# Performance work log

Measured on AMD Instinct MI355X. Metric: run time of the kernel, lower is better.

## Reference

```python
import jax, jax.numpy as jnp
import numpy as np

B, N, C, H, AD, HID = 2, 1024, 768, 12, 8, 3072
SCALE = (C // H) ** -0.5


def setup_inputs() -> dict:
    key = jax.random.key(0)
    ks = jax.random.split(key, 32)
    inp = {}
    for i in range(5):
        inp[f"x{i}"] = jax.random.normal(ks[i], (B, N, C), jnp.float32)
    def w(i, shape, s=0.02):
        return jax.random.normal(ks[i], shape, jnp.float32) * s
    inp.update({
        "ln1_g": jnp.ones((C,), jnp.float32), "ln1_b": jnp.zeros((C,), jnp.float32),
        "ln2_g": jnp.ones((C,), jnp.float32), "ln2_b": jnp.zeros((C,), jnp.float32),
        "qkv_w": w(5, (C, 3 * C)), "qkv_b": jnp.zeros((3 * C,), jnp.float32),
        "proj_w": w(6, (C, C)), "proj_b": jnp.zeros((C,), jnp.float32),
        "fc1_w": w(7, (C, HID)), "fc1_b": jnp.zeros((HID,), jnp.float32),
        "fc2_w": w(8, (HID, C)), "fc2_b": jnp.zeros((C,), jnp.float32),
        "at_dw": w(9, (C, AD)), "at_db": jnp.zeros((AD,), jnp.float32),
        "at_mw": w(10, (AD, AD)), "at_mb": jnp.zeros((AD,), jnp.float32),
        "at_uw": w(11, (AD, C)), "at_ub": jnp.zeros((C,), jnp.float32),
        "a2_dw": w(12, (C, AD)), "a2_db": jnp.zeros((AD,), jnp.float32),
        "a2_mw": w(13, (AD, AD)), "a2_mb": jnp.zeros((AD,), jnp.float32),
        "a2_uw": w(14, (AD, C)), "a2_ub": jnp.zeros((C,), jnp.float32),
    })
    return inp


def _ln(x, g, b, eps=1e-5):
    mu = x.mean(-1, keepdims=True)
    xc = x - mu
    var = (xc * xc).mean(-1, keepdims=True)
    return xc * jax.lax.rsqrt(var + eps) * g + b


def _adapter(x, dw, db, mw, mb, uw, ub):
    h = x @ dw + db          # bottleneck down [., AD]
    h = h @ mw + mb          # mid
    return h @ uw + ub       # up back to C


def _attn(x, qkv_w, qkv_b, proj_w, proj_b):
    # x: [S, B, N, C] (streams folded in leading axis)
    s, b, n, c = x.shape
    qkv = (x @ qkv_w + qkv_b).reshape(s, b, n, 3, H, c // H)
    q, k, v = jnp.moveaxis(qkv, 3, 0)            # each [S,B,N,H,D]
    scores = jnp.einsum('sbnhd,sbmhd->sbhnm', q * SCALE, k)  # fp32; clamp is a no-op
    p = jax.nn.softmax(scores, axis=-1)
    o = jnp.einsum('sbhnm,sbmhd->sbnhd', p, v).reshape(s, b, n, c)
    return o @ proj_w + proj_b


def reference(x0, x1, x2, x3, x4,
              ln1_g, ln1_b, ln2_g, ln2_b,
              qkv_w, qkv_b, proj_w, proj_b,
              fc1_w, fc1_b, fc2_w, fc2_b,
              at_dw, at_db, at_mw, at_mb, at_uw, at_ub,
              a2_dw, a2_db, a2_mw, a2_mb, a2_uw, a2_ub):
    xs = jnp.stack([x0, x1, x2, x3, x4])          # [5,B,N,C]
    n1 = _ln(xs, ln1_g, ln1_b)
    a1 = _adapter(n1, at_dw, at_db, at_mw, at_mb, at_uw, at_ub)
    ao = _attn(n1, qkv_w, qkv_b, proj_w, proj_b)
    # cross-stream residuals: x01=a1[0], x12=a1[1], ..., x10=a1[1], x21=a1[2], ...
    y0 = xs[0] + ao[0] + a1[1]
    y1 = xs[1] + ao[1] + a1[0] + a1[2]
    y2 = xs[2] + ao[2] + a1[1] + a1[3]
    y3 = xs[3] + ao[3] + a1[2] + a1[4]
    y4 = xs[4] + ao[4] + a1[3]
    ys = jnp.stack([y0, y1, y2, y3, y4])
    a2 = _adapter(_ln(ys, ln1_g, ln1_b), a2_dw, a2_db, a2_mw, a2_mb, a2_uw, a2_ub)
    h = _ln(ys, ln2_g, ln2_b) @ fc1_w + fc1_b
    m = jax.nn.gelu(h, approximate=False) @ fc2_w + fc2_b
    z0 = ys[0] + m[0] + a2[1]
    z1 = ys[1] + m[1] + a2[0] + a2[2]
    z2 = ys[2] + m[2] + a2[1] + a2[3]
    z3 = ys[3] + m[3] + a2[2] + a2[4]
    z4 = ys[4] + m[4] + a2[3]
    return jnp.stack([z0, z1, z2, z3, z4])        # [5,B,N,C]
```

## Files before the change

kernel.cpp:

```cpp
#include <hip/hip_runtime.h>
#include <math.h>

typedef __bf16 bf16;
typedef __attribute__((ext_vector_type(8))) __bf16 bf16x8;
typedef __attribute__((ext_vector_type(4))) __bf16 bf16x4;
typedef __attribute__((ext_vector_type(4))) float f32x4;
typedef __attribute__((ext_vector_type(16))) float f32x16;

#define TOK   10240
#define CD    768
#define NQKV  2304
#define NHID  3072
#define SEQ   1024
#define NH    12

__device__ __forceinline__ f32x4 mfma16(bf16x8 a, bf16x8 b, f32x4 c) {
  return __builtin_amdgcn_mfma_f32_16x16x32_bf16(a, b, c, 0, 0, 0);
}
__device__ __forceinline__ f32x16 mfma32(bf16x8 a, bf16x8 b, f32x16 c) {
  return __builtin_amdgcn_mfma_f32_32x32x16_bf16(a, b, c, 0, 0, 0);
}

__device__ __forceinline__ void gload16(const void* g, void* l) {
  __builtin_amdgcn_global_load_lds(
      (const __attribute__((address_space(1))) void*)g,
      (__attribute__((address_space(3))) void*)l, 16, 0, 0);
}

__device__ __forceinline__ unsigned pack2(bf16 a, bf16 b) {
  union { unsigned short u[2]; unsigned v; } x;
  x.u[0] = __builtin_bit_cast(unsigned short, a);
  x.u[1] = __builtin_bit_cast(unsigned short, b);
  return x.v;
}

__device__ __forceinline__ f32x4 b4tof(const bf16* p) {
  bf16x4 v = *(const bf16x4*)p;
  f32x4 r;
#pragma unroll
  for (int j = 0; j < 4; ++j) r[j] = (float)v[j];
  return r;
}

__device__ __forceinline__ float fast_gelu(float v) {
  float u = 0.7978845608f * (v + 0.044715f * v * v * v);
  float e = __expf(fminf(2.f * u, 30.f));
  return 0.5f * v * (1.f + (e - 1.f) / (e + 1.f));
}

__global__ __launch_bounds__(256) void transpose_to_bf16(
    const float* __restrict__ in, bf16* __restrict__ out, int K, int N) {
  __shared__ float tile[32][33];
  const int bn = blockIdx.x * 32, bk = blockIdx.y * 32;
  const int r = threadIdx.x >> 5, c = threadIdx.x & 31;
#pragma unroll
  for (int i = 0; i < 4; ++i)
    tile[r + 8 * i][c] = in[(size_t)(bk + r + 8 * i) * N + bn + c];
  __syncthreads();
#pragma unroll
  for (int i = 0; i < 4; ++i)
    out[(size_t)(bn + r + 8 * i) * K + bk + c] = (bf16)tile[c][r + 8 * i];
}

__global__ __launch_bounds__(256) void ln5_kernel(
    const float* __restrict__ x0, const float* __restrict__ x1,
    const float* __restrict__ x2, const float* __restrict__ x3,
    const float* __restrict__ x4, const float* __restrict__ g,
    const float* __restrict__ b, bf16* __restrict__ out) {
  const int w = threadIdx.x >> 6, lane = threadIdx.x & 63;
  const int row = blockIdx.x * 4 + w;
  const int s = row >> 11, rem = row & 2047;
  const float* xp;
  switch (s) {
    case 0: xp = x0; break; case 1: xp = x1; break; case 2: xp = x2; break;
    case 3: xp = x3; break; default: xp = x4; break;
  }
  const f32x4* xr = (const f32x4*)(xp + (size_t)rem * CD);
  f32x4 v[3];
#pragma unroll
  for (int i = 0; i < 3; ++i) v[i] = xr[lane + 64 * i];
  float sum = 0.f;
#pragma unroll
  for (int i = 0; i < 3; ++i)
#pragma unroll
    for (int j = 0; j < 4; ++j) sum += v[i][j];
#pragma unroll
  for (int m = 32; m >= 1; m >>= 1) sum += __shfl_xor(sum, m);
  const float mu = sum * (1.f / 768.f);
  float vs = 0.f;
#pragma unroll
  for (int i = 0; i < 3; ++i)
#pragma unroll
    for (int j = 0; j < 4; ++j) { float d = v[i][j] - mu; vs += d * d; }
#pragma unroll
  for (int m = 32; m >= 1; m >>= 1) vs += __shfl_xor(vs, m);
  const float rstd = rsqrtf(vs * (1.f / 768.f) + 1e-5f);
  const f32x4* gp = (const f32x4*)g;
  const f32x4* bp = (const f32x4*)b;
  bf16* orow = out + (size_t)row * CD;
#pragma unroll
  for (int i = 0; i < 3; ++i) {
    const int c4 = lane + 64 * i;
    f32x4 gg = gp[c4], bb = bp[c4];
    bf16x4 o;
#pragma unroll
    for (int j = 0; j < 4; ++j)
      o[j] = (bf16)((v[i][j] - mu) * rstd * gg[j] + bb[j]);
    *(bf16x4*)(orow + c4 * 4) = o;
  }
}

__global__ __launch_bounds__(256) void fuse_res_ln(
    const float* __restrict__ x0, const float* __restrict__ x1,
    const float* __restrict__ x2, const float* __restrict__ x3,
    const float* __restrict__ x4, const float* __restrict__ add,
    const bf16* __restrict__ a, float* __restrict__ ys,
    const float* __restrict__ g1, const float* __restrict__ b1,
    const float* __restrict__ g2, const float* __restrict__ b2,
    bf16* __restrict__ o1, bf16* __restrict__ o2) {
  const int w = threadIdx.x >> 6, lane = threadIdx.x & 63;
  const int row = blockIdx.x * 4 + w;
  const int s = row >> 11, rem = row & 2047;
  const float* xp;
  switch (s) {
    case 0: xp = x0; break; case 1: xp = x1; break; case 2: xp = x2; break;
    case 3: xp = x3; break; default: xp = x4; break;
  }
  const f32x4* xr = (const f32x4*)(xp + (size_t)rem * CD);
  const f32x4* ar = (const f32x4*)(add + (size_t)row * CD);
  const bf16* am = a + (size_t)(row - 2048) * CD;
  const bf16* ap = a + (size_t)(row + 2048) * CD;
  f32x4 v[3];
#pragma unroll
  for (int i = 0; i < 3; ++i) {
    const int c4 = lane + 64 * i;
    f32x4 t = xr[c4] + ar[c4];
    if (s > 0) t += b4tof(am + c4 * 4);
    if (s < 4) t += b4tof(ap + c4 * 4);
    v[i] = t;
  }
  f32x4* yr = (f32x4*)(ys + (size_t)row * CD);
#pragma unroll
  for (int i = 0; i < 3; ++i) yr[lane + 64 * i] = v[i];

  float sum = 0.f;
#pragma unroll
  for (int i = 0; i < 3; ++i)
#pragma unroll
    for (int j = 0; j < 4; ++j) sum += v[i][j];
#pragma unroll
  for (int m = 32; m >= 1; m >>= 1) sum += __shfl_xor(sum, m);
  const float mu = sum * (1.f / 768.f);
  float vs = 0.f;
#pragma unroll
  for (int i = 0; i < 3; ++i)
#pragma unroll
    for (int j = 0; j < 4; ++j) { float d = v[i][j] - mu; vs += d * d; }
#pragma unroll
  for (int m = 32; m >= 1; m >>= 1) vs += __shfl_xor(vs, m);
  const float rstd = rsqrtf(vs * (1.f / 768.f) + 1e-5f);
  bf16* r1 = o1 + (size_t)row * CD;
  bf16* r2 = o2 + (size_t)row * CD;
#pragma unroll
  for (int i = 0; i < 3; ++i) {
    const int c4 = lane + 64 * i;
    f32x4 gg1 = ((const f32x4*)g1)[c4], bb1 = ((const f32x4*)b1)[c4];
    f32x4 gg2 = ((const f32x4*)g2)[c4], bb2 = ((const f32x4*)b2)[c4];
    bf16x4 oa, ob;
#pragma unroll
    for (int j = 0; j < 4; ++j) {
      float n = (v[i][j] - mu) * rstd;
      oa[j] = (bf16)(n * gg1[j] + bb1[j]);
      ob[j] = (bf16)(n * gg2[j] + bb2[j]);
    }
    *(bf16x4*)(r1 + c4 * 4) = oa;
    *(bf16x4*)(r2 + c4 * 4) = ob;
  }
}

#define GBAR() __builtin_amdgcn_s_barrier()

#define LOADA(MH, BUF)                                                      \
  _Pragma("unroll") for (int m_ = 0; m_ < 4; ++m_) {                        \
    af[m_][0] =                                                             \
        *(const bf16x8*)&As[BUF][((MH)*128 + arow + m_ * 16) * 64 + ach0];  \
    af[m_][1] =                                                             \
        *(const bf16x8*)&As[BUF][((MH)*128 + arow + m_ * 16) * 64 + ach1];  \
  }

#define LOADB(DST, NH, BUF)                                                 \
  _Pragma("unroll") for (int n_ = 0; n_ < 2; ++n_) {                        \
    DST[n_][0] =                                                            \
        *(const bf16x8*)&Bs[BUF][(brow + (NH)*32 + n_ * 16) * 64 + ach0];   \
    DST[n_][1] =                                                            \
        *(const bf16x8*)&Bs[BUF][(brow + (NH)*32 + n_ * 16) * 64 + ach1];   \
  }

#define MFMA_PH(MH, NH, BF)                                                 \
  __builtin_amdgcn_s_setprio(1);                                            \
  _Pragma("unroll") for (int m_ = 0; m_ < 4; ++m_)                          \
  _Pragma("unroll") for (int n_ = 0; n_ < 2; ++n_) {                        \
    acc[(MH)*4 + m_][(NH)*2 + n_] =                                         \
        mfma16(af[m_][0], BF[n_][0], acc[(MH)*4 + m_][(NH)*2 + n_]);        \
    acc[(MH)*4 + m_][(NH)*2 + n_] =                                         \
        mfma16(af[m_][1], BF[n_][1], acc[(MH)*4 + m_][(NH)*2 + n_]);        \
  }                                                                         \
  __builtin_amdgcn_s_setprio(0);

template <int EPI>
__global__ __launch_bounds__(512, 2) void gemm256(
    const bf16* __restrict__ A, const bf16* __restrict__ Bt,
    const float* __restrict__ bias, void* __restrict__ Cout, int N, int Klen,
    int ldk, int nbn, int bpk, size_t kpstride) {
  __shared__ bf16 As[2][16384];
  __shared__ bf16 Bs[2][16384];
  const int t = threadIdx.x, lane = t & 63, w = t >> 6;
  const int wm = w >> 2, wn = w & 3;

  const int chunkg = gridDim.x >> 3;
  const int wg = (blockIdx.x & 7) * chunkg + (blockIdx.x >> 3);
  const int kp = wg / bpk, rem = wg % bpk;
  const int bm = rem / nbn, bn = rem % nbn;

  f32x4 acc[8][4] = {};

  const int srow = t >> 3;
  const int scol = ((t & 7) ^ (srow & 7)) << 3;
  const size_t koff = (size_t)kp * Klen;
  const bf16* Ab = A + (size_t)(bm * 256 + srow) * ldk + koff + scol;
  const bf16* Bb = Bt + (size_t)(bn * 256 + srow) * ldk + koff + scol;
  const size_t r64 = (size_t)64 * ldk;

  auto stage_a = [&](int buf, int h, int kt) {
    const bf16* g = Ab + (size_t)h * 128 * ldk + (size_t)kt * 64;
    gload16(g, &As[buf][h * 8192 + w * 512]);
    gload16(g + r64, &As[buf][h * 8192 + 4096 + w * 512]);
  };
  auto stage_b = [&](int buf, int h, int kt) {
    const bf16* g = Bb + (size_t)h * 128 * ldk + (size_t)kt * 64;
    gload16(g, &Bs[buf][h * 8192 + w * 512]);
    gload16(g + r64, &Bs[buf][h * 8192 + 4096 + w * 512]);
  };

  const int arow = wm * 64 + (lane & 15);
  const int brow = wn * 64 + (lane & 15);
  const int ach0 = (((lane >> 4) + 0) ^ (lane & 7)) << 3;
  const int ach1 = (((lane >> 4) + 4) ^ (lane & 7)) << 3;

  stage_a(0, 0, 0); stage_b(0, 0, 0); stage_b(0, 1, 0); stage_a(0, 1, 0);
  stage_a(1, 0, 1); stage_b(1, 0, 1);
  asm volatile("s_waitcnt vmcnt(4)" ::: "memory");
  GBAR();

  const int NT = Klen >> 6, NI = NT >> 1;
  bf16x8 af[4][2], bf0[2][2], bf1[2][2];

  for (int j = 0; j < NI; ++j) {
    const int tA = 2 * j, tB = 2 * j + 1;
    const bool notlast = (j + 1 < NI);

    LOADA(0, 0);
    LOADB(bf0, 0, 0);
    stage_b(1, 1, tB);
    GBAR();
    MFMA_PH(0, 0, bf0);
    GBAR();
    LOADB(bf1, 1, 0);
    stage_a(1, 1, tB);
    GBAR();
    MFMA_PH(0, 1, bf1);
    GBAR();
    LOADA(1, 0);
    if (notlast) stage_a(0, 0, tA + 2);
    GBAR();
    MFMA_PH(1, 0, bf0);
    GBAR();
    if (notlast) {
      stage_b(0, 0, tA + 2);
      asm volatile("s_waitcnt vmcnt(4)" ::: "memory");
    } else {
      asm volatile("s_waitcnt vmcnt(0)" ::: "memory");
    }
    GBAR();
    MFMA_PH(1, 1, bf1);
    GBAR();

    LOADA(0, 1);
    LOADB(bf0, 0, 1);
    if (notlast) stage_b(0, 1, tA + 2);
    GBAR();
    MFMA_PH(0, 0, bf0);
    GBAR();
    LOADB(bf1, 1, 1);
    if (notlast) stage_a(0, 1, tA + 2);
    GBAR();
    MFMA_PH(0, 1, bf1);
    GBAR();
    LOADA(1, 1);
    if (notlast) stage_a(1, 0, tB + 2);
    GBAR();
    MFMA_PH(1, 0, bf0);
    GBAR();
    if (notlast) {
      stage_b(1, 0, tB + 2);
      asm volatile("s_waitcnt vmcnt(4)" ::: "memory");
    }
    GBAR();
    MFMA_PH(1, 1, bf1);
    GBAR();
  }

#pragma unroll
  for (int am = 0; am < 8; ++am) {
    const int grow0 =
        bm * 256 + (am >> 2) * 128 + wm * 64 + (am & 3) * 16 + (lane >> 4) * 4;
#pragma unroll
    for (int an = 0; an < 4; ++an) {
      const int gcol = bn * 256 + wn * 64 + an * 16 + (lane & 15);
      const float bv = (kp == 0) ? bias[gcol] : 0.f;
#pragma unroll
      for (int r = 0; r < 4; ++r) {
        float v = acc[am][an][r] + bv;
        if (EPI == 2) v = fast_gelu(v);
        const size_t idx = (size_t)(grow0 + r) * N + gcol + kp * kpstride;
        if (EPI == 0) ((float*)Cout)[idx] = v;
        else ((bf16*)Cout)[idx] = (bf16)v;
      }
    }
  }
}

__global__ __launch_bounds__(256, 3) void attn_v2(
    const bf16* __restrict__ qkv, bf16* __restrict__ obuf) {
  __shared__ bf16 Ks[2][4096];
  __shared__ bf16 Vt[2][4096];
  const int t = threadIdx.x, lane = t & 63, w = t >> 6;
  const int g = lane >> 5, q32 = lane & 31, rq7 = q32 & 7;

  const int xcd = blockIdx.x & 7, slot = blockIdx.x >> 3;
  const int work = xcd * 120 + slot;
  const int sbh = work >> 3, qt = work & 7;
  const int sb = sbh / NH, h = sbh % NH;
  const size_t tokbase = (size_t)sb * SEQ;
  const int qoff = h * 64, koff = CD + h * 64, voff = 2 * CD + h * 64;

  const int qrow = qt * 128 + w * 32 + q32;
  bf16x8 qf[4];
  {
    const bf16* qp = qkv + (tokbase + qrow) * NQKV + qoff + g * 8;
#pragma unroll
    for (int kd = 0; kd < 4; ++kd) {
      bf16x8 v = *(const bf16x8*)(qp + kd * 16);
#pragma unroll
      for (int j = 0; j < 8; ++j) v[j] = (bf16)((float)v[j] * 0.125f);
      qf[kd] = v;
    }
  }

  const int skv1 = t >> 3, sc1 = (t & 7) ^ (skv1 & 7);
  const int skv2 = (t + 256) >> 3, sc2 = (t & 7) ^ (skv2 & 7);
  const int vkv0 = 2 * (t & 31);
  const int vd0 = 8 * (t >> 5);
  const int c0 = (vkv0 & 51) | ((vkv0 & 4) << 1) | ((vkv0 & 8) >> 1);
  const int vchunk = c0 >> 3, vsub = c0 & 7;
  const bf16* kbase = qkv + tokbase * NQKV + koff;
  const bf16* vbase = qkv + tokbase * NQKV + voff;

  {
    const bf16* kb0 = kbase;
    gload16(kb0 + (size_t)skv1 * NQKV + sc1 * 8, &Ks[0][w * 512]);
    gload16(kb0 + (size_t)skv2 * NQKV + sc2 * 8, &Ks[0][2048 + w * 512]);
    const bf16* vp = vbase + (size_t)vkv0 * NQKV + vd0;
    bf16x8 r0 = *(const bf16x8*)vp;
    bf16x8 r1 = *(const bf16x8*)(vp + NQKV);
#pragma unroll
    for (int j = 0; j < 8; ++j) {
      const int d = vd0 + j;
      *(unsigned*)&Vt[0][d * 64 + ((vchunk ^ j) << 3) + vsub] =
          pack2(r0[j], r1[j]);
    }
  }
  __syncthreads();

  float m_run = -1e30f, l_run = 0.f;
  f32x16 oT0 = {}, oT1 = {};
  int cur = 0;

  for (int kt = 0; kt < 16; ++kt) {
    bf16x8 nv0, nv1;
    if (kt < 15) {
      const bf16* vp = vbase + (size_t)((kt + 1) * 64 + vkv0) * NQKV + vd0;
      nv0 = *(const bf16x8*)vp;
      nv1 = *(const bf16x8*)(vp + NQKV);
      const bf16* kb0 = kbase + (size_t)(kt + 1) * 64 * NQKV;
      gload16(kb0 + (size_t)skv1 * NQKV + sc1 * 8, &Ks[cur ^ 1][w * 512]);
      gload16(kb0 + (size_t)skv2 * NQKV + sc2 * 8,
              &Ks[cur ^ 1][2048 + w * 512]);
    }

    f32x16 sT0 = {}, sT1 = {};
#pragma unroll
    for (int kd = 0; kd < 4; ++kd) {
      bf16x8 kf0 =
          *(const bf16x8*)&Ks[cur][q32 * 64 + (((2 * kd + g) ^ rq7) << 3)];
      bf16x8 kf1 = *(const bf16x8*)&Ks[cur][(32 + q32) * 64 +
                                            (((2 * kd + g) ^ rq7) << 3)];
      sT0 = mfma32(kf0, qf[kd], sT0);
      sT1 = mfma32(kf1, qf[kd], sT1);
    }

    float mt = sT0[0];
#pragma unroll
    for (int r = 1; r < 16; ++r) mt = fmaxf(mt, sT0[r]);
#pragma unroll
    for (int r = 0; r < 16; ++r) mt = fmaxf(mt, sT1[r]);
    mt = fmaxf(mt, __shfl_xor(mt, 32));
    const float mnew = fmaxf(m_run, mt);
    const float alpha = __expf(m_run - mnew);
    m_run = mnew;
    float rs = 0.f;
#pragma unroll
    for (int r = 0; r < 16; ++r) {
      sT0[r] = __expf(sT0[r] - mnew);
      rs += sT0[r];
    }
#pragma unroll
    for (int r = 0; r < 16; ++r) {
      sT1[r] = __expf(sT1[r] - mnew);
      rs += sT1[r];
    }
    rs += __shfl_xor(rs, 32);
    l_run = l_run * alpha + rs;
#pragma unroll
    for (int r = 0; r < 16; ++r) { oT0[r] *= alpha; oT1[r] *= alpha; }

    bf16x8 pa[4];
#pragma unroll
    for (int hh = 0; hh < 2; ++hh)
#pragma unroll
      for (int j = 0; j < 8; ++j) {
        pa[hh][j] = (bf16)sT0[8 * hh + j];
        pa[2 + hh][j] = (bf16)sT1[8 * hh + j];
      }

#pragma unroll
    for (int ks = 0; ks < 4; ++ks) {
      bf16x8 vf0 =
          *(const bf16x8*)&Vt[cur][q32 * 64 + (((2 * ks + g) ^ rq7) << 3)];
      bf16x8 vf1 = *(const bf16x8*)&Vt[cur][(32 + q32) * 64 +
                                            (((2 * ks + g) ^ rq7) << 3)];
      oT0 = mfma32(vf0, pa[ks], oT0);
      oT1 = mfma32(vf1, pa[ks], oT1);
    }

    if (kt < 15) {
#pragma unroll
      for (int j = 0; j < 8; ++j) {
        const int d = vd0 + j;
        *(unsigned*)&Vt[cur ^ 1][d * 64 + ((vchunk ^ j) << 3) + vsub] =
            pack2(nv0[j], nv1[j]);
      }
    }
    __syncthreads();
    cur ^= 1;
  }

  const float rl = 1.f / l_run;
  bf16* orow = obuf + (tokbase + qrow) * CD + h * 64;
#pragma unroll
  for (int m = 0; m < 4; ++m) {
    bf16x4 o0, o1;
#pragma unroll
    for (int r = 0; r < 4; ++r) {
      o0[r] = (bf16)(oT0[4 * m + r] * rl);
      o1[r] = (bf16)(oT1[4 * m + r] * rl);
    }
    *(bf16x4*)(orow + 8 * m + 4 * g) = o0;
    *(bf16x4*)(orow + 32 + 8 * m + 4 * g) = o1;
  }
}

__global__ __launch_bounds__(256) void adapter_kernel(
    const bf16* __restrict__ X, const float* __restrict__ dw,
    const float* __restrict__ db, const float* __restrict__ mw,
    const float* __restrict__ mb, const float* __restrict__ uw,
    const float* __restrict__ ub, bf16* __restrict__ out) {
  const int tok = blockIdx.x * 4 + (threadIdx.x >> 6);
  const int lane = threadIdx.x & 63;
  const bf16* xr = X + (size_t)tok * CD;
  float xv[12];
#pragma unroll
  for (int i = 0; i < 12; ++i) xv[i] = (float)xr[lane + 64 * i];
  float h1[8] = {0, 0, 0, 0, 0, 0, 0, 0};
#pragma unroll
  for (int i = 0; i < 12; ++i) {
    const f32x4* dr = (const f32x4*)(dw + (size_t)(lane + 64 * i) * 8);
    f32x4 d0 = dr[0], d1 = dr[1];
#pragma unroll
    for (int j = 0; j < 4; ++j) {
      h1[j] += xv[i] * d0[j];
      h1[4 + j] += xv[i] * d1[j];
    }
  }
#pragma unroll
  for (int m = 1; m < 64; m <<= 1)
#pragma unroll
    for (int j = 0; j < 8; ++j) h1[j] += __shfl_xor(h1[j], m);
#pragma unroll
  for (int j = 0; j < 8; ++j) h1[j] += db[j];
  float h2[8];
#pragma unroll
  for (int k = 0; k < 8; ++k) {
    float v = mb[k];
#pragma unroll
    for (int j = 0; j < 8; ++j) v += h1[j] * mw[j * 8 + k];
    h2[k] = v;
  }
#pragma unroll
  for (int i = 0; i < 12; ++i) {
    const int c = lane + 64 * i;
    float v = ub[c];
#pragma unroll
    for (int k = 0; k < 8; ++k) v += h2[k] * uw[k * CD + c];
    out[(size_t)tok * CD + c] = (bf16)v;
  }
}

__global__ __launch_bounds__(256) void cross_residual(
    const float* __restrict__ ys, const bf16* __restrict__ m01,
    const bf16* __restrict__ a, float* __restrict__ out) {
  const int s = blockIdx.y;
  const size_t i = (size_t)blockIdx.x * 256 + threadIdx.x;
  const size_t spitch = (size_t)2048 * 768 / 4;
  const size_t sb = (size_t)s * spitch;
  const size_t mstride = (size_t)TOK * CD / 4;
  f32x4 v = ((const f32x4*)ys)[sb + i];
  v += b4tof(m01 + (sb + i) * 4);
  v += b4tof(m01 + (mstride + sb + i) * 4);
  if (s > 0) v += b4tof(a + (sb - spitch + i) * 4);
  if (s < 4) v += b4tof(a + (sb + spitch + i) * 4);
  ((f32x4*)out)[sb + i] = v;
}

#define OFF_WTQKV  ((size_t)0)
#define OFF_WTPROJ ((size_t)3538944)
#define OFF_WTFC1  ((size_t)4718592)
#define OFF_WTFC2  ((size_t)9437184)
#define OFF_N1     ((size_t)14155776)
#define OFF_BIG    ((size_t)29884416)
#define OFF_OBUF   ((size_t)77070336)
#define OFF_AOM    ((size_t)92798976)
#define OFF_A12    ((size_t)124256256)
#define OFF_YS     ((size_t)155713536)
#define OFF_L2Y    ((size_t)187170816)

extern "C" void kernel_launch(void* const* d_in, const int* in_sizes, int n_in,
                              void* d_out, int out_size, void* d_ws,
                              size_t ws_size, hipStream_t stream) {
  const float* x0 = (const float*)d_in[0];
  const float* x1 = (const float*)d_in[1];
  const float* x2 = (const float*)d_in[2];
  const float* x3 = (const float*)d_in[3];
  const float* x4 = (const float*)d_in[4];
  const float* ln1_g = (const float*)d_in[5];
  const float* ln1_b = (const float*)d_in[6];
  const float* ln2_g = (const float*)d_in[7];
  const float* ln2_b = (const float*)d_in[8];
  const float* qkv_w = (const float*)d_in[9];
  const float* qkv_b = (const float*)d_in[10];
  const float* proj_w = (const float*)d_in[11];
  const float* proj_b = (const float*)d_in[12];
  const float* fc1_w = (const float*)d_in[13];
  const float* fc1_b = (const float*)d_in[14];
  const float* fc2_w = (const float*)d_in[15];
  const float* fc2_b = (const float*)d_in[16];
  const float* at_dw = (const float*)d_in[17];
  const float* at_db = (const float*)d_in[18];
  const float* at_mw = (const float*)d_in[19];
  const float* at_mb = (const float*)d_in[20];
  const float* at_uw = (const float*)d_in[21];
  const float* at_ub = (const float*)d_in[22];
  const float* a2_dw = (const float*)d_in[23];
  const float* a2_db = (const float*)d_in[24];
  const float* a2_mw = (const float*)d_in[25];
  const float* a2_mb = (const float*)d_in[26];
  const float* a2_uw = (const float*)d_in[27];
  const float* a2_ub = (const float*)d_in[28];

  char* ws = (char*)d_ws;
  bf16* wt_qkv = (bf16*)(ws + OFF_WTQKV);
  bf16* wt_proj = (bf16*)(ws + OFF_WTPROJ);
  bf16* wt_fc1 = (bf16*)(ws + OFF_WTFC1);
  bf16* wt_fc2 = (bf16*)(ws + OFF_WTFC2);
  bf16* n1 = (bf16*)(ws + OFF_N1);
  bf16* qkvb = (bf16*)(ws + OFF_BIG);
  bf16* obuf = (bf16*)(ws + OFF_OBUF);
  float* aof = (float*)(ws + OFF_AOM);
  bf16* mbuf = (bf16*)(ws + OFF_AOM);
  bf16* a12 = (bf16*)(ws + OFF_A12);
  float* ysb = (float*)(ws + OFF_YS);
  bf16* l2y = (bf16*)(ws + OFF_L2Y);

  const dim3 b256(256);
  const dim3 b512(512);

  transpose_to_bf16<<<dim3(72, 24), b256, 0, stream>>>(qkv_w, wt_qkv, 768, 2304);
  transpose_to_bf16<<<dim3(24, 24), b256, 0, stream>>>(proj_w, wt_proj, 768, 768);
  transpose_to_bf16<<<dim3(96, 24), b256, 0, stream>>>(fc1_w, wt_fc1, 768, 3072);
  transpose_to_bf16<<<dim3(24, 96), b256, 0, stream>>>(fc2_w, wt_fc2, 3072, 768);

  ln5_kernel<<<2560, b256, 0, stream>>>(x0, x1, x2, x3, x4, ln1_g, ln1_b, n1);

  gemm256<1><<<360, b512, 0, stream>>>(n1, wt_qkv, qkv_b, qkvb, NQKV, 768, 768,
                                       9, 360, 0);

  adapter_kernel<<<2560, b256, 0, stream>>>(n1, at_dw, at_db, at_mw, at_mb,
                                            at_uw, at_ub, a12);

  attn_v2<<<960, b256, 0, stream>>>(qkvb, obuf);

  gemm256<0><<<120, b512, 0, stream>>>(obuf, wt_proj, proj_b, aof, CD, 768,
                                       768, 3, 120, 0);

  fuse_res_ln<<<2560, b256, 0, stream>>>(x0, x1, x2, x3, x4, aof, a12, ysb,
                                         ln1_g, ln1_b, ln2_g, ln2_b, n1, l2y);

  adapter_kernel<<<2560, b256, 0, stream>>>(n1, a2_dw, a2_db, a2_mw, a2_mb,
                                            a2_uw, a2_ub, a12);

  gemm256<2><<<480, b512, 0, stream>>>(l2y, wt_fc1, fc1_b, qkvb, NHID, 768,
                                       768, 12, 480, 0);

  gemm256<1><<<240, b512, 0, stream>>>(qkvb, wt_fc2, fc2_b, mbuf, CD, 1536,
                                       3072, 3, 120, (size_t)TOK * CD);

  cross_residual<<<dim3(1536, 5), b256, 0, stream>>>(ysb, mbuf, a12,
                                                     (float*)d_out);
}
```

Measured before the change: 382.9 us.

## Simplify GEMM to K=32 double-buffered loop and split-K the projection GEMM

Replaces the hand-interleaved 8-phase GEMM main loop, which used K=64 tiles and many barriers, with a simpler loop using K=32 tiles and a double buffer. Each step loads all A and B fragments, waits, prefetches the tile two steps ahead, then issues 32 MFMAs, and LDS use is halved. The output projection GEMM now uses split-K over 240 blocks and writes two bf16 partial outputs instead of one fp32 output. The fused residual+LN kernel sums the two bf16 partials, which should fill more CUs but adds bf16 rounding on the projection output. The simpler loop also risks less overlap between loads and MFMA.

```diff
diff --git a/kernel.cpp b/kernel.cpp
--- a/kernel.cpp
+++ b/kernel.cpp
@@ -113,7 +113,7 @@
 __global__ __launch_bounds__(256) void fuse_res_ln(
     const float* __restrict__ x0, const float* __restrict__ x1,
     const float* __restrict__ x2, const float* __restrict__ x3,
-    const float* __restrict__ x4, const float* __restrict__ add,
+    const float* __restrict__ x4, const bf16* __restrict__ m01,
     const bf16* __restrict__ a, float* __restrict__ ys,
     const float* __restrict__ g1, const float* __restrict__ b1,
     const float* __restrict__ g2, const float* __restrict__ b2,
@@ -127,14 +127,15 @@
     case 3: xp = x3; break; default: xp = x4; break;
   }
   const f32x4* xr = (const f32x4*)(xp + (size_t)rem * CD);
-  const f32x4* ar = (const f32x4*)(add + (size_t)row * CD);
+  const bf16* p0 = m01 + (size_t)row * CD;
+  const bf16* p1 = m01 + (size_t)TOK * CD + (size_t)row * CD;
   const bf16* am = a + (size_t)(row - 2048) * CD;
   const bf16* ap = a + (size_t)(row + 2048) * CD;
   f32x4 v[3];
 #pragma unroll
   for (int i = 0; i < 3; ++i) {
     const int c4 = lane + 64 * i;
-    f32x4 t = xr[c4] + ar[c4];
+    f32x4 t = xr[c4] + b4tof(p0 + c4 * 4) + b4tof(p1 + c4 * 4);
     if (s > 0) t += b4tof(am + c4 * 4);
     if (s < 4) t += b4tof(ap + c4 * 4);
     v[i] = t;
@@ -178,42 +179,13 @@
   }
 }
 
-#define GBAR() __builtin_amdgcn_s_barrier()
-
-#define LOADA(MH, BUF)                                                      \
-  _Pragma("unroll") for (int m_ = 0; m_ < 4; ++m_) {                        \
-    af[m_][0] =                                                             \
-        *(const bf16x8*)&As[BUF][((MH)*128 + arow + m_ * 16) * 64 + ach0];  \
-    af[m_][1] =                                                             \
-        *(const bf16x8*)&As[BUF][((MH)*128 + arow + m_ * 16) * 64 + ach1];  \
-  }
-
-#define LOADB(DST, NH, BUF)                                                 \
-  _Pragma("unroll") for (int n_ = 0; n_ < 2; ++n_) {                        \
-    DST[n_][0] =                                                            \
-        *(const bf16x8*)&Bs[BUF][(brow + (NH)*32 + n_ * 16) * 64 + ach0];   \
-    DST[n_][1] =                                                            \
-        *(const bf16x8*)&Bs[BUF][(brow + (NH)*32 + n_ * 16) * 64 + ach1];   \
-  }
-
-#define MFMA_PH(MH, NH, BF)                                                 \
-  __builtin_amdgcn_s_setprio(1);                                            \
-  _Pragma("unroll") for (int m_ = 0; m_ < 4; ++m_)                          \
-  _Pragma("unroll") for (int n_ = 0; n_ < 2; ++n_) {                        \
-    acc[(MH)*4 + m_][(NH)*2 + n_] =                                         \
-        mfma16(af[m_][0], BF[n_][0], acc[(MH)*4 + m_][(NH)*2 + n_]);        \
-    acc[(MH)*4 + m_][(NH)*2 + n_] =                                         \
-        mfma16(af[m_][1], BF[n_][1], acc[(MH)*4 + m_][(NH)*2 + n_]);        \
-  }                                                                         \
-  __builtin_amdgcn_s_setprio(0);
-
 template <int EPI>
 __global__ __launch_bounds__(512, 2) void gemm256(
     const bf16* __restrict__ A, const bf16* __restrict__ Bt,
     const float* __restrict__ bias, void* __restrict__ Cout, int N, int Klen,
     int ldk, int nbn, int bpk, size_t kpstride) {
-  __shared__ bf16 As[2][16384];
-  __shared__ bf16 Bs[2][16384];
+  __shared__ bf16 As[2][8192];
+  __shared__ bf16 Bs[2][8192];
   const int t = threadIdx.x, lane = t & 63, w = t >> 6;
   const int wm = w >> 2, wn = w & 3;
 
@@ -224,103 +196,70 @@
 
   f32x4 acc[8][4] = {};
 
-  const int srow = t >> 3;
-  const int scol = ((t & 7) ^ (srow & 7)) << 3;
+  const int srow = t >> 2;
+  const int scol = ((t & 3) ^ ((srow >> 1) & 3)) << 3;
   const size_t koff = (size_t)kp * Klen;
   const bf16* Ab = A + (size_t)(bm * 256 + srow) * ldk + koff + scol;
   const bf16* Bb = Bt + (size_t)(bn * 256 + srow) * ldk + koff + scol;
-  const size_t r64 = (size_t)64 * ldk;
-
-  auto stage_a = [&](int buf, int h, int kt) {
-    const bf16* g = Ab + (size_t)h * 128 * ldk + (size_t)kt * 64;
-    gload16(g, &As[buf][h * 8192 + w * 512]);
-    gload16(g + r64, &As[buf][h * 8192 + 4096 + w * 512]);
+  const size_t r128 = (size_t)128 * ldk;
+
+  auto stage = [&](int buf, int kt) {
+    const bf16* ga = Ab + (size_t)kt * 32;
+    const bf16* gb = Bb + (size_t)kt * 32;
+    gload16(ga, &As[buf][w * 512]);
+    gload16(ga + r128, &As[buf][4096 + w * 512]);
+    gload16(gb, &Bs[buf][w * 512]);
+    gload16(gb + r128, &Bs[buf][4096 + w * 512]);
   };
-  auto stage_b = [&](int buf, int h, int kt) {
-    const bf16* g = Bb + (size_t)h * 128 * ldk + (size_t)kt * 64;
-    gload16(g, &Bs[buf][h * 8192 + w * 512]);
-    gload16(g + r64, &Bs[buf][h * 8192 + 4096 + w * 512]);
-  };
-
-  const int arow = wm * 64 + (lane & 15);
+
+  const int arow = wm * 128 + (lane & 15);
   const int brow = wn * 64 + (lane & 15);
-  const int ach0 = (((lane >> 4) + 0) ^ (lane & 7)) << 3;
-  const int ach1 = (((lane >> 4) + 4) ^ (lane & 7)) << 3;
-
-  stage_a(0, 0, 0); stage_b(0, 0, 0); stage_b(0, 1, 0); stage_a(0, 1, 0);
-  stage_a(1, 0, 1); stage_b(1, 0, 1);
+  const int achn = (((lane >> 4) ^ ((lane >> 1) & 3)) << 3);
+
+  stage(0, 0);
+  stage(1, 1);
   asm volatile("s_waitcnt vmcnt(4)" ::: "memory");
-  GBAR();
-
-  const int NT = Klen >> 6, NI = NT >> 1;
-  bf16x8 af[4][2], bf0[2][2], bf1[2][2];
-
-  for (int j = 0; j < NI; ++j) {
-    const int tA = 2 * j, tB = 2 * j + 1;
-    const bool notlast = (j + 1 < NI);
-
-    LOADA(0, 0);
-    LOADB(bf0, 0, 0);
-    stage_b(1, 1, tB);
-    GBAR();
-    MFMA_PH(0, 0, bf0);
-    GBAR();
-    LOADB(bf1, 1, 0);
-    stage_a(1, 1, tB);
-    GBAR();
-    MFMA_PH(0, 1, bf1);
-    GBAR();
-    LOADA(1, 0);
-    if (notlast) stage_a(0, 0, tA + 2);
-    GBAR();
-    MFMA_PH(1, 0, bf0);
-    GBAR();
-    if (notlast) {
-      stage_b(0, 0, tA + 2);
+  __builtin_amdgcn_s_barrier();
+
+  const int NT = Klen >> 5;
+  bf16x8 af[8], bfr[4];
+
+  for (int kt = 0; kt < NT; ++kt) {
+    const int buf = kt & 1;
+#pragma unroll
+    for (int m_ = 0; m_ < 8; ++m_)
+      af[m_] = *(const bf16x8*)&As[buf][(arow + m_ * 16) * 32 + achn];
+#pragma unroll
+    for (int n_ = 0; n_ < 4; ++n_)
+      bfr[n_] = *(const bf16x8*)&Bs[buf][(brow + n_ * 16) * 32 + achn];
+    asm volatile("s_waitcnt lgkmcnt(0)" ::: "memory");
+    __builtin_amdgcn_s_barrier();
+    if (kt + 2 < NT) {
+      stage(buf, kt + 2);
       asm volatile("s_waitcnt vmcnt(4)" ::: "memory");
     } else {
       asm volatile("s_waitcnt vmcnt(0)" ::: "memory");
     }
-    GBAR();
-    MFMA_PH(1, 1, bf1);
-    GBAR();
-
-    LOADA(0, 1);
-    LOADB(bf0, 0, 1);
-    if (notlast) stage_b(0, 1, tA + 2);
-    GBAR();
-    MFMA_PH(0, 0, bf0);
-    GBAR();
-    LOADB(bf1, 1, 1);
-    if (notlast) stage_a(0, 1, tA + 2);
-    GBAR();
-    MFMA_PH(0, 1, bf1);
-    GBAR();
-    LOADA(1, 1);
-    if (notlast) stage_a(1, 0, tB + 2);
-    GBAR();
-    MFMA_PH(1, 0, bf0);
-    GBAR();
-    if (notlast) {
-      stage_b(1, 0, tB + 2);
-      asm volatile("s_waitcnt vmcnt(4)" ::: "memory");
-    }
-    GBAR();
-    MFMA_PH(1, 1, bf1);
-    GBAR();
-  }
-
-#pragma unroll
-  for (int am = 0; am < 8; ++am) {
-    const int grow0 =
-        bm * 256 + (am >> 2) * 128 + wm * 64 + (am & 3) * 16 + (lane >> 4) * 4;
-#pragma unroll
-    for (int an = 0; an < 4; ++an) {
-      const int gcol = bn * 256 + wn * 64 + an * 16 + (lane & 15);
+    __builtin_amdgcn_s_barrier();
+    __builtin_amdgcn_s_setprio(1);
+#pragma unroll
+    for (int m_ = 0; m_ < 8; ++m_)
+#pragma unroll
+      for (int n_ = 0; n_ < 4; ++n_)
+        acc[m_][n_] = mfma16(af[m_], bfr[n_], acc[m_][n_]);
+    __builtin_amdgcn_s_setprio(0);
+  }
+
+#pragma unroll
+  for (int m_ = 0; m_ < 8; ++m_) {
+    const int grow0 = bm * 256 + wm * 128 + m_ * 16 + (lane >> 4) * 4;
+#pragma unroll
+    for (int n_ = 0; n_ < 4; ++n_) {
+      const int gcol = bn * 256 + wn * 64 + n_ * 16 + (lane & 15);
       const float bv = (kp == 0) ? bias[gcol] : 0.f;
 #pragma unroll
       for (int r = 0; r < 4; ++r) {
-        float v = acc[am][an][r] + bv;
+        float v = acc[m_][n_][r] + bv;
         if (EPI == 2) v = fast_gelu(v);
         const size_t idx = (size_t)(grow0 + r) * N + gcol + kp * kpstride;
         if (EPI == 0) ((float*)Cout)[idx] = v;
@@ -595,7 +534,6 @@
   bf16* n1 = (bf16*)(ws + OFF_N1);
   bf16* qkvb = (bf16*)(ws + OFF_BIG);
   bf16* obuf = (bf16*)(ws + OFF_OBUF);
-  float* aof = (float*)(ws + OFF_AOM);
   bf16* mbuf = (bf16*)(ws + OFF_AOM);
   bf16* a12 = (bf16*)(ws + OFF_A12);
   float* ysb = (float*)(ws + OFF_YS);
@@ -619,10 +557,10 @@
 
   attn_v2<<<960, b256, 0, stream>>>(qkvb, obuf);
 
-  gemm256<0><<<120, b512, 0, stream>>>(obuf, wt_proj, proj_b, aof, CD, 768,
-                                       768, 3, 120, 0);
-
-  fuse_res_ln<<<2560, b256, 0, stream>>>(x0, x1, x2, x3, x4, aof, a12, ysb,
+  gemm256<1><<<240, b512, 0, stream>>>(obuf, wt_proj, proj_b, mbuf, CD, 384,
+                                       768, 3, 120, (size_t)TOK * CD);
+
+  fuse_res_ln<<<2560, b256, 0, stream>>>(x0, x1, x2, x3, x4, mbuf, a12, ysb,
                                          ln1_g, ln1_b, ln2_g, ln2_b, n1, l2y);
 
   adapter_kernel<<<2560, b256, 0, stream>>>(n1, a2_dw, a2_db, a2_mw, a2_mb,
```

After: 389.2 us. No clear change (+1.6%).
